# Optimization experiments

Measured on AMD Instinct MI355X. Metric: run time of the kernel, lower is better.

The kernel has to match this reference:

```python
import jax, jax.numpy as jnp
import numpy as np

N = 100000          # nodes (edges-as-nodes in ChiENN)
CIRCLE = 8          # circle_size
D_IN = 128
D_OUT = 128
K = 2               # k_neighbors -> padding = K - 1 = 1
PAD = K - 1


def setup_inputs() -> dict:
    key = jax.random.key(0)
    ks = jax.random.split(key, 8)
    x = jax.random.normal(ks[0], (N, D_IN), dtype=jnp.float32)
    # circle_index: per-row first `length` entries are valid node ids, tail is -1 padding
    lengths = jax.random.randint(ks[1], (N,), 0, CIRCLE + 1)  # 0..CIRCLE
    idx = jax.random.randint(ks[2], (N, CIRCLE), 0, N)
    pos = jnp.arange(CIRCLE)[None, :]
    circle_index = jnp.where(pos < lengths[:, None], idx, -1).astype(jnp.int64)
    s = 1.0 / np.sqrt(D_IN)
    w1 = jax.random.uniform(ks[3], (D_IN, D_OUT), jnp.float32, -s, s)
    b1 = jnp.zeros((D_OUT,), jnp.float32)
    w2 = jax.random.uniform(ks[4], (D_IN, D_OUT), jnp.float32, -s, s)
    b2 = jnp.zeros((D_OUT,), jnp.float32)
    sf = 1.0 / np.sqrt(D_OUT)
    wf = jax.random.uniform(ks[5], (D_OUT, D_OUT), jnp.float32, -sf, sf)
    bf = jnp.zeros((D_OUT,), jnp.float32)
    return {"x": x, "w1": w1, "b1": b1, "w2": w2, "b2": b2,
            "wf": wf, "bf": bf, "circle_index": circle_index}


def reference(x, w1, b1, w2, b2, wf, bf, circle_index):
    n, circle_size = circle_index.shape
    agg_id = 0.0  # aggregation_id_element for 'add'

    # per-shift embeddings of node features, each with a zero row prepended (index 0 = padding)
    embs = [x @ w1 + b1, x @ w2 + b2]                       # each [N, D]
    d = embs[0].shape[-1]
    zero_row = jnp.zeros((1, d), embs[0].dtype)
    embs = [jnp.concatenate([zero_row, e], axis=0) for e in embs]  # [N+1, D]

    mask_sum = jnp.sum(circle_index == -1, axis=-1)          # [N]
    in_degree = circle_size - mask_sum - PAD
    in_degree = jnp.where(mask_sum == circle_size, 0, in_degree)

    ci = circle_index.reshape(-1) + 1                        # [N*circle]  (-1 -> 0 = zero row)
    L = ci.shape[0]
    ci = jnp.concatenate([ci, jnp.zeros((PAD,), ci.dtype)])

    shifted = []
    for i, e in enumerate(embs):
        se = e[ci[i:i + L]]                                  # [L, D] circular-shifted gather
        # mask rows whose node in-degree <= shift i
        m = jnp.repeat(in_degree <= i, circle_size)[:, None]  # [L, 1]
        shifted.append(jnp.where(m, agg_id, se))
    msg = jnp.sum(jnp.stack(shifted, axis=-2), axis=-2)      # 'add' aggregation, [L, D]
    msg = msg.reshape(n, circle_size, d)

    msg_mask = jnp.arange(1, circle_size + 1)[None, :] <= in_degree[:, None]
    msg = msg[:, :-PAD, :]                                   # drop circular padding slots
    msg_mask = msg_mask[:, :-PAD]
    msg = jnp.where(msg_mask[..., None], msg, 0.0)
    msg = msg @ wf + bf                                      # final_embedding (Linear)
    return msg, msg_mask
```

## Files before the change

### kernel.cpp

```cpp
#include <hip/hip_runtime.h>
#include <stdint.h>

typedef short bf16x8 __attribute__((ext_vector_type(8)));
typedef float f32x4  __attribute__((ext_vector_type(4)));

__device__ __forceinline__ unsigned short f2bf(float f) {
    unsigned int u = __float_as_uint(f);
    u += 0x7FFFu + ((u >> 16) & 1u);
    return (unsigned short)(u >> 16);
}
__device__ __forceinline__ float bf2f(unsigned short h) {
    return __uint_as_float(((unsigned int)h) << 16);
}

__global__ void fuse_weights(const float* __restrict__ w1, const float* __restrict__ b1,
                             const float* __restrict__ w2, const float* __restrict__ b2,
                             const float* __restrict__ wf,
                             unsigned short* __restrict__ wcT,
                             float* __restrict__ cb)
{
    int mat = blockIdx.x / 129;
    int kk  = blockIdx.x % 129;
    int c   = threadIdx.x;
    const float* w = (mat == 0) ? w1 : w2;
    const float* b = (mat == 0) ? b1 : b2;
    float acc = 0.f;
    if (kk < 128) {
        #pragma unroll 8
        for (int j = 0; j < 128; ++j) acc += w[kk * 128 + j] * wf[j * 128 + c];
        wcT[mat * 16384 + c * 128 + kk] = f2bf(acc);
    } else {
        #pragma unroll 8
        for (int j = 0; j < 128; ++j) acc += b[j] * wf[j * 128 + c];
        cb[mat * 128 + c] = acc;
    }
}

__global__ __launch_bounds__(512, 4) void gemm_g(
    const float* __restrict__ x, const unsigned short* __restrict__ wcT,
    const float* __restrict__ cb, unsigned short* __restrict__ g,
    int nrows, int rpb)
{
    __shared__ uint4 ldsw[4096];

    int tid  = threadIdx.x;
    int lane = tid & 63;
    int wid  = tid >> 6;
    int rbase = blockIdx.x * rpb;
    int rend  = rbase + rpb; if (rend > nrows) rend = nrows;
    int r0   = rbase + wid * 32;
    int lrow = lane & 15;
    int kg   = lane >> 4;
    int swz  = (lrow & 7) << 4;

    const uint4* w4 = (const uint4*)wcT;
    #pragma unroll
    for (int i = 0; i < 8; ++i) {
        int idx = tid + i * 512;
        uint4 v = w4[idx];
        int b   = idx << 4;
        int sb  = b ^ (((b >> 8) & 7) << 4);
        ldsw[sb >> 4] = v;
    }

    bf16x8 xf[2][4];
    #pragma unroll
    for (int t = 0; t < 2; ++t) {
        int row = r0 + t * 16 + lrow;
        bool v  = row < rend;
        #pragma unroll
        for (int ks = 0; ks < 4; ++ks) {
            int k0 = ks * 32 + kg * 8;
            float4 p0 = v ? *(const float4*)(x + (size_t)row * 128 + k0)     : float4{0,0,0,0};
            float4 p1 = v ? *(const float4*)(x + (size_t)row * 128 + k0 + 4) : float4{0,0,0,0};
            bf16x8 f;
            f[0] = (short)f2bf(p0.x); f[1] = (short)f2bf(p0.y);
            f[2] = (short)f2bf(p0.z); f[3] = (short)f2bf(p0.w);
            f[4] = (short)f2bf(p1.x); f[5] = (short)f2bf(p1.y);
            f[6] = (short)f2bf(p1.z); f[7] = (short)f2bf(p1.w);
            xf[t][ks] = f;
        }
    }

    __syncthreads();
    if (r0 >= rend) return;

    const char* lbase = (const char*)ldsw;
    #pragma unroll
    for (int mat = 0; mat < 2; ++mat) {
        unsigned short* gm = g + (size_t)mat * nrows * 128;
        int mb = mat * 32768;
        #pragma unroll 2
        for (int c = 0; c < 8; ++c) {
            int colb = mb + (c * 16 + lrow) * 256 + kg * 16;
            bf16x8 wfr[4];
            #pragma unroll
            for (int ks = 0; ks < 4; ++ks)
                wfr[ks] = *(const bf16x8*)(lbase + ((colb + ks * 64) ^ swz));
            f32x4 acc[2];
            #pragma unroll
            for (int t = 0; t < 2; ++t) acc[t] = f32x4{0,0,0,0};
            #pragma unroll
            for (int ks = 0; ks < 4; ++ks) {
                #pragma unroll
                for (int t = 0; t < 2; ++t)
                    acc[t] = __builtin_amdgcn_mfma_f32_16x16x32_bf16(wfr[ks], xf[t][ks], acc[t], 0,0,0);
            }
            float4 bias = *(const float4*)(cb + mat * 128 + c * 16 + kg * 4);
            #pragma unroll
            for (int t = 0; t < 2; ++t) {
                int xrow = r0 + t * 16 + lrow;
                if (xrow < rend) {
                    ushort4 o;
                    o.x = f2bf(acc[t][0] + bias.x); o.y = f2bf(acc[t][1] + bias.y);
                    o.z = f2bf(acc[t][2] + bias.z); o.w = f2bf(acc[t][3] + bias.w);
                    *(ushort4*)(gm + (size_t)xrow * 128 + c * 16 + kg * 4) = o;
                }
            }
        }
    }
}

__global__ __launch_bounds__(256) void gather_out(
    const int* __restrict__ ci, const unsigned short* __restrict__ g,
    const float* __restrict__ bfv, float* __restrict__ out,
    float* __restrict__ maskout, int nnodes)
{
    int n    = (int)((blockIdx.x * blockDim.x + threadIdx.x) >> 6);
    int lane = threadIdx.x & 63;
    if (n >= nnodes) return;

    int civ = ci[n * 8 + (lane & 7)];
    unsigned long long bal = __ballot(civ == -1);
    int cnt = __popcll(bal & 0xFFull);
    int deg = (cnt == 8) ? 0 : (7 - cnt);

    int half = lane >> 5;
    int hl   = lane & 31;
    int d4   = hl * 4;
    float4 bfd = *(const float4*)(bfv + d4);
    const unsigned short* g1 = g;
    const unsigned short* g2 = g + (size_t)nnodes * 128;
    bool two = (deg >= 2);

    uint2 va[4], vb[4];
    #pragma unroll
    for (int c = 0; c < 4; ++c) {
        va[c] = uint2{0u, 0u};
        vb[c] = uint2{0u, 0u};
        if (2 * c < deg) {
            int r  = 2 * c + half;
            int i0 = __shfl(civ, r);
            int i1 = __shfl(civ, r + 1);
            bool m = (r < deg);
            va[c] = m          ? *(const uint2*)(g1 + (size_t)i0 * 128 + d4) : uint2{0u, 0u};
            vb[c] = (m && two) ? *(const uint2*)(g2 + (size_t)i1 * 128 + d4) : uint2{0u, 0u};
        }
    }

    size_t base = (size_t)n * 896;
    #pragma unroll
    for (int c = 0; c < 4; ++c) {
        f32x4 o;
        o[0] = bfd.x + bf2f((unsigned short)(va[c].x & 0xFFFFu)) + bf2f((unsigned short)(vb[c].x & 0xFFFFu));
        o[1] = bfd.y + bf2f((unsigned short)(va[c].x >> 16))     + bf2f((unsigned short)(vb[c].x >> 16));
        o[2] = bfd.z + bf2f((unsigned short)(va[c].y & 0xFFFFu)) + bf2f((unsigned short)(vb[c].y & 0xFFFFu));
        o[3] = bfd.w + bf2f((unsigned short)(va[c].y >> 16))     + bf2f((unsigned short)(vb[c].y >> 16));
        if (c < 3)
            __builtin_nontemporal_store(o, (f32x4*)(out + base + c * 256 + lane * 4));
        else if (half == 0)
            __builtin_nontemporal_store(o, (f32x4*)(out + base + 768 + hl * 4));
    }
    if (lane < 7)
        __builtin_nontemporal_store((lane < deg) ? 1.0f : 0.0f, maskout + n * 7 + lane);
}

extern "C" void kernel_launch(void* const* d_in, const int* in_sizes, int n_in,
                              void* d_out, int out_size, void* d_ws, size_t ws_size,
                              hipStream_t stream) {
    const float* x   = (const float*)d_in[0];
    const float* w1  = (const float*)d_in[1];
    const float* b1  = (const float*)d_in[2];
    const float* w2  = (const float*)d_in[3];
    const float* b2  = (const float*)d_in[4];
    const float* wf  = (const float*)d_in[5];
    const float* bfv = (const float*)d_in[6];
    const int*   ci  = (const int*)d_in[7];

    int nrows = in_sizes[0] / 128;

    size_t gbytes = (size_t)2 * nrows * 128 * 2;
    unsigned short* g   = (unsigned short*)d_ws;
    unsigned short* wcT = (unsigned short*)((char*)d_ws + ((gbytes + 255) & ~(size_t)255));
    float*          cb  = (float*)((char*)wcT + 2 * 128 * 128 * 2);

    fuse_weights<<<2 * 129, 128, 0, stream>>>(w1, b1, w2, b2, wf, wcT, cb);

    int nblkB = 512;
    int rpb   = (nrows + nblkB - 1) / nblkB;
    gemm_g<<<nblkB, 512, 0, stream>>>(x, wcT, cb, g, nrows, rpb);

    int rows = nrows * 7;
    int cblk = (nrows * 64 + 255) / 256;
    float* out = (float*)d_out;
    gather_out<<<cblk, 256, 0, stream>>>(ci, g, bfv, out, out + (size_t)rows * 128, nrows);
}
```

Before: 108.5 us.

## Fuse weight-folding kernel into GEMM via grid-wide atomic barrier

Moves the weight-folding step (W1@Wf, W2@Wf and the folded biases) into the GEMM kernel. The first 65 blocks compute it, then every block waits at a global atomic barrier before loading the folded weights into LDS. This removes one kernel launch and its serialization gap, but adds a memset launch, a spin barrier that needs all 512 blocks resident at once, and an idle wait for most blocks while a few do the fold.

```diff
diff --git a/kernel.cpp b/kernel.cpp
--- a/kernel.cpp
+++ b/kernel.cpp
@@ -13,45 +13,61 @@
     return __uint_as_float(((unsigned int)h) << 16);
 }
 
-__global__ void fuse_weights(const float* __restrict__ w1, const float* __restrict__ b1,
-                             const float* __restrict__ w2, const float* __restrict__ b2,
-                             const float* __restrict__ wf,
-                             unsigned short* __restrict__ wcT,
-                             float* __restrict__ cb)
-{
-    int mat = blockIdx.x / 129;
-    int kk  = blockIdx.x % 129;
-    int c   = threadIdx.x;
-    const float* w = (mat == 0) ? w1 : w2;
-    const float* b = (mat == 0) ? b1 : b2;
-    float acc = 0.f;
-    if (kk < 128) {
-        #pragma unroll 8
-        for (int j = 0; j < 128; ++j) acc += w[kk * 128 + j] * wf[j * 128 + c];
-        wcT[mat * 16384 + c * 128 + kk] = f2bf(acc);
-    } else {
-        #pragma unroll 8
-        for (int j = 0; j < 128; ++j) acc += b[j] * wf[j * 128 + c];
-        cb[mat * 128 + c] = acc;
-    }
-}
-
-__global__ __launch_bounds__(512, 4) void gemm_g(
-    const float* __restrict__ x, const unsigned short* __restrict__ wcT,
-    const float* __restrict__ cb, unsigned short* __restrict__ g,
-    int nrows, int rpb)
+__global__ __launch_bounds__(512, 4) void fgemm(
+    const float* __restrict__ x,
+    const float* __restrict__ w1, const float* __restrict__ b1,
+    const float* __restrict__ w2, const float* __restrict__ b2,
+    const float* __restrict__ wf,
+    unsigned short* __restrict__ wcT, float* __restrict__ cb,
+    unsigned short* __restrict__ g,
+    int nrows, int rpb, int nblk, unsigned* __restrict__ bar)
 {
     __shared__ uint4 ldsw[4096];
 
     int tid  = threadIdx.x;
+    int bid  = blockIdx.x;
     int lane = tid & 63;
     int wid  = tid >> 6;
-    int rbase = blockIdx.x * rpb;
+
+    {
+        int tg = bid * 512 + tid;
+        if (tg < 258 * 128) {
+            int c   = tg & 127;
+            int job = tg >> 7;
+            int mat = (job >= 129) ? 1 : 0;
+            int kk  = job - mat * 129;
+            const float* w = mat ? w2 : w1;
+            const float* b = mat ? b2 : b1;
+            float acc = 0.f;
+            if (kk < 128) {
+                #pragma unroll 8
+                for (int j = 0; j < 128; ++j) acc += w[kk * 128 + j] * wf[j * 128 + c];
+                wcT[mat * 16384 + c * 128 + kk] = f2bf(acc);
+            } else {
+                #pragma unroll 8
+                for (int j = 0; j < 128; ++j) acc += b[j] * wf[j * 128 + c];
+                cb[mat * 128 + c] = acc;
+            }
+        }
+    }
+
+    __syncthreads();
+    if (tid == 0) {
+        __threadfence();
+        atomicAdd(bar, 1u);
+        while (__hip_atomic_load(bar, __ATOMIC_RELAXED, __HIP_MEMORY_SCOPE_AGENT)
+               < (unsigned)nblk)
+            __builtin_amdgcn_s_sleep(1);
+        __threadfence();
+    }
+    __syncthreads();
+
+    int rbase = bid * rpb;
     int rend  = rbase + rpb; if (rend > nrows) rend = nrows;
-    int r0   = rbase + wid * 32;
-    int lrow = lane & 15;
-    int kg   = lane >> 4;
-    int swz  = (lrow & 7) << 4;
+    int r0    = rbase + wid * 32;
+    int lrow  = lane & 15;
+    int kg    = lane >> 4;
+    int swz   = (lrow & 7) << 4;
 
     const uint4* w4 = (const uint4*)wcT;
     #pragma unroll
@@ -193,12 +209,14 @@
     unsigned short* g   = (unsigned short*)d_ws;
     unsigned short* wcT = (unsigned short*)((char*)d_ws + ((gbytes + 255) & ~(size_t)255));
     float*          cb  = (float*)((char*)wcT + 2 * 128 * 128 * 2);
-
-    fuse_weights<<<2 * 129, 128, 0, stream>>>(w1, b1, w2, b2, wf, wcT, cb);
+    unsigned*       bar = (unsigned*)((char*)cb + 1024);
+
+    hipMemsetAsync(bar, 0, 64, stream);
 
     int nblkB = 512;
     int rpb   = (nrows + nblkB - 1) / nblkB;
-    gemm_g<<<nblkB, 512, 0, stream>>>(x, wcT, cb, g, nrows, rpb);
+    fgemm<<<nblkB, 512, 0, stream>>>(x, w1, b1, w2, b2, wf, wcT, cb, g,
+                                     nrows, rpb, nblkB, bar);
 
     int rows = nrows * 7;
     int cblk = (nrows * 64 + 255) / 256;
```

Measured after the change: 140.7 us. +29.7%, slower.
